# Kernel tuning notes

Measured on AMD Instinct MI355X. Metric: run time of the kernel, lower is better.

The kernel has to match this reference:

```python
import jax, jax.numpy as jnp
import numpy as np

B, L = 2048, 4096
ALPHA = 1.0   # cfgs['metric']['alpha']
BETA = 0.5    # cfgs['metric']['beta']
ENC = 0.0     # cfgs['metric']['enc'] (encoder=None -> term is 0)


def _peak_mask(x, distance):
    """GPU-friendly equivalent of scipy.signal.find_peaks(x, distance=d):
    strict local maxima + min-distance suppression via window-max (NMS).
    x: [B, L] -> bool mask [B, L]."""
    interior = (x[:, 1:-1] > x[:, :-2]) & (x[:, 1:-1] > x[:, 2:])
    local_max = jnp.pad(interior, ((0, 0), (1, 1)))
    w = 2 * distance - 1
    pooled = jax.lax.reduce_window(x, -jnp.inf, jax.lax.max,
                                   (1, w), (1, 1), 'SAME')
    return local_max & (x >= pooled)


def _forward(in_signal, ref_signal):
    # plain MSE over the whole batch
    mse_loss = jnp.mean((in_signal - ref_signal) ** 2)

    # cosine similarity, mean over batch
    dot = jnp.sum(in_signal * ref_signal, axis=-1)
    na = jnp.linalg.norm(in_signal, axis=-1)
    nb = jnp.linalg.norm(ref_signal, axis=-1)
    cosine_similarity = jnp.mean(dot / (na * nb))

    # peak detection: distance=20 for count comparison (custom_error branch)
    m20_in = _peak_mask(in_signal, 20)
    m20_ref = _peak_mask(ref_signal, 20)
    n_in = jnp.sum(m20_in, axis=-1)
    n_ref = jnp.sum(m20_ref, axis=-1)

    # peak-to-peak error: distance=10 peaks; MSE between peak-masked signals
    # (fixed-shape, position-aligned stand-in for get_peaks_info_of_segments)
    m10_in = _peak_mask(in_signal, 10)
    m10_ref = _peak_mask(ref_signal, 10)
    pk_in = jnp.where(m10_in, in_signal, 0.0)
    pk_ref = jnp.where(m10_ref, ref_signal, 0.0)
    p2p_i = jnp.mean((pk_in - pk_ref) ** 2, axis=-1)   # [B]

    mse_i = jnp.mean((in_signal - ref_signal) ** 2, axis=-1)  # [B]

    custom_loss = jnp.sum(jnp.where(n_in != n_ref, mse_i * ALPHA, p2p_i * BETA))
    p2p_loss = jnp.sum(p2p_i)

    total_loss = mse_loss + custom_loss  # + ENC * 0 (encoder is None)
    return jnp.stack([total_loss, cosine_similarity, p2p_loss, mse_loss])


def setup_inputs() -> dict:
    key = jax.random.key(0)
    k1, k2 = jax.random.split(key)
    in_signal = jax.random.normal(k1, (B, L), dtype=jnp.float32)
    ref_signal = jax.random.normal(k2, (B, L), dtype=jnp.float32)
    return {"in_signal": in_signal, "ref_signal": ref_signal}


def reference(in_signal, ref_signal):
    return _forward(in_signal, ref_signal)
```

## Files before the change

### kernel.cpp

```cpp
#include <hip/hip_runtime.h>
#include <math.h>

#define LL 4096
#define BB 2048
#define NT 512
#define CH 8
#define ALPHA 1.0f
#define BETA 0.5f
#define NEG_INF (-__builtin_inff())
#define POS_INF (__builtin_inff())

#define SPSZ 4672
#define OFS(d) ((d) + ((d) >> 3) + 27)

template <int CTRL, int RM>
__device__ __forceinline__ float dpp_addf(float v) {
    int s = __builtin_amdgcn_update_dpp(0, __float_as_int(v), CTRL, RM, 0xf, true);
    return v + __int_as_float(s);
}
__device__ __forceinline__ float wredf(float v) {
    v = dpp_addf<0x111, 0xf>(v);
    v = dpp_addf<0x112, 0xf>(v);
    v = dpp_addf<0x114, 0xf>(v);
    v = dpp_addf<0x118, 0xf>(v);
    v = dpp_addf<0x142, 0xa>(v);
    v = dpp_addf<0x143, 0xc>(v);
    return v;
}

__global__ __launch_bounds__(NT, 6) void row_kernel(const float* __restrict__ gA,
                                                    const float* __restrict__ gB,
                                                    float4* __restrict__ rowout) {
    __shared__ float sS[SPSZ];
    __shared__ float sP[SPSZ];
    __shared__ float4 red4[NT / 64][2];

    const int b = blockIdx.x;
    const int t = threadIdx.x;
    float* const Sb = sS + 9 * t;
    float* const Pb = sP + 9 * t;
    const float* rowA = gA + (size_t)b * LL;
    const float* rowB = gB + (size_t)b * LL;

    float xA[CH], xB[CH];
    {
        const float4* a4 = (const float4*)rowA;
        const float4* b4 = (const float4*)rowB;
#pragma unroll
        for (int k = 0; k < CH / 4; ++k) {
            float4 v = a4[t * (CH / 4) + k];
            xA[4 * k + 0] = v.x; xA[4 * k + 1] = v.y; xA[4 * k + 2] = v.z; xA[4 * k + 3] = v.w;
            float4 u = b4[t * (CH / 4) + k];
            xB[4 * k + 0] = u.x; xB[4 * k + 1] = u.y; xB[4 * k + 2] = u.z; xB[4 * k + 3] = u.w;
        }
    }

    {
        float se = 0.f, dt = 0.f, na = 0.f, nb = 0.f;
#pragma unroll
        for (int j = 0; j < CH; ++j) {
            float d = xA[j] - xB[j];
            se += d * d;
            dt += xA[j] * xB[j];
            na += xA[j] * xA[j];
            nb += xB[j] * xB[j];
        }
        se = wredf(se); dt = wredf(dt); na = wredf(na); nb = wredf(nb);
        if ((t & 63) == 63) red4[t >> 6][0] = make_float4(se, dt, na, nb);
    }

    if (t < 24) {
        int i = t - 24;
        int p = i + (i >> 3) + 27;
        sS[p] = NEG_INF; sP[p] = NEG_INF;
    } else if (t >= NT - 24) {
        int i = LL + (t - (NT - 24));
        int p = i + (i >> 3) + 27;
        sS[p] = NEG_INF; sP[p] = NEG_INF;
    }

    auto process = [&](const float (&x)[CH], int& cnt20, unsigned& m10) {
        float pp[CH], ss[CH];
        pp[0] = x[0];
#pragma unroll
        for (int j = 1; j < CH; ++j) pp[j] = fmaxf(pp[j - 1], x[j]);
        ss[CH - 1] = x[CH - 1];
#pragma unroll
        for (int j = CH - 2; j >= 0; --j) ss[j] = fmaxf(ss[j + 1], x[j]);
#pragma unroll
        for (int j = 0; j < CH; ++j) {
            Pb[j + 27] = pp[j];
            Sb[j + 27] = ss[j];
        }
        const float cmax = pp[CH - 1];
        __syncthreads();

        const float Cm2 = Pb[OFS(-9)];
        const float Cm1 = Pb[OFS(-1)];
        const float Cp1 = Pb[OFS(15)];
        const float Cp2 = Pb[OFS(23)];
        const float f1 = fmaxf(Cm1, cmax);
        const float f2 = fmaxf(cmax, Cp1);
        const float g2 = fmaxf(f1, Cp1);
        const float g1 = fmaxf(g2, Cm2);
        const float g3 = fmaxf(g2, Cp2);
        const float xm1 = (t == 0)      ? POS_INF : Sb[OFS(-1)];
        const float xp1 = (t == NT - 1) ? POS_INF : Pb[OFS(8)];

        cnt20 = 0; m10 = 0u;
#pragma unroll
        for (int j = 0; j < CH; ++j) {
            float xi = x[j];
            float xl = (j > 0)      ? x[j - 1] : xm1;
            float xr = (j < CH - 1) ? x[j + 1] : xp1;
            bool lm = (xi > xl) && (xi > xr);
            float a19 = Sb[OFS(j - 9)];
            float b19 = Pb[OFS(j + 9)];
            float a39 = Sb[OFS(j - 19)];
            float b39 = Pb[OFS(j + 19)];
            float mid19 = (j == 0) ? f1 : ((j == CH - 1) ? f2 : cmax);
            float mid39 = (j <= 2) ? g1 : ((j <= 4) ? g2 : g3);
            float p19 = fmaxf(fmaxf(a19, b19), mid19);
            float p39 = fmaxf(fmaxf(a39, b39), mid39);
            if (lm && xi >= p19) m10 |= (1u << j);
            if (lm && xi >= p39) cnt20++;
        }
    };

    int cntA, cntB;
    unsigned mA, mB;
    process(xA, cntA, mA);
    __syncthreads();
    process(xB, cntB, mB);

    float p2p = 0.f;
#pragma unroll
    for (int j = 0; j < CH; ++j) {
        float av = ((mA >> j) & 1u) ? xA[j] : 0.f;
        float bv = ((mB >> j) & 1u) ? xB[j] : 0.f;
        float d = av - bv;
        p2p += d * d;
    }

    p2p = wredf(p2p);
    float cc = wredf((float)(cntA * 4096 + cntB));
    if ((t & 63) == 63) red4[t >> 6][1] = make_float4(p2p, cc, 0.f, 0.f);
    __syncthreads();

    if (t == 0) {
        float s0 = 0, s1 = 0, s2 = 0, s3 = 0, s4 = 0, s5 = 0;
#pragma unroll
        for (int i = 0; i < NT / 64; ++i) {
            float4 u = red4[i][0];
            float4 v = red4[i][1];
            s0 += u.x; s1 += u.y; s2 += u.z; s3 += u.w;
            s4 += v.x; s5 += v.y;
        }
        int packed = (int)s5;
        int ca = packed >> 12;
        int cb = packed & 4095;
        float mse_i = s0 / (float)LL;
        float cos_i = s1 / (sqrtf(s2) * sqrtf(s3));
        float p2p_i = s4 / (float)LL;
        float custom_i = (ca != cb) ? (mse_i * ALPHA) : (p2p_i * BETA);
        rowout[b] = make_float4(mse_i, cos_i, p2p_i, custom_i);
    }
}

__global__ __launch_bounds__(256) void reduce_kernel(const float4* __restrict__ rows,
                                                     float* __restrict__ out) {
    __shared__ float red[4][4];
    float sx = 0.f, sy = 0.f, sz = 0.f, sw = 0.f;
    for (int r = threadIdx.x; r < BB; r += 256) {
        float4 v = rows[r];
        sx += v.x; sy += v.y; sz += v.z; sw += v.w;
    }
    sx = wredf(sx); sy = wredf(sy); sz = wredf(sz); sw = wredf(sw);
    int w = threadIdx.x >> 6, lane = threadIdx.x & 63;
    if (lane == 63) { red[w][0] = sx; red[w][1] = sy; red[w][2] = sz; red[w][3] = sw; }
    __syncthreads();
    if (threadIdx.x == 0) {
        float ax = 0, ay = 0, az = 0, aw = 0;
        for (int i = 0; i < 4; ++i) {
            ax += red[i][0]; ay += red[i][1]; az += red[i][2]; aw += red[i][3];
        }
        float mse = ax / (float)BB;
        out[0] = mse + aw;
        out[1] = ay / (float)BB;
        out[2] = az;
        out[3] = mse;
    }
}

extern "C" void kernel_launch(void* const* d_in, const int* in_sizes, int n_in,
                              void* d_out, int out_size, void* d_ws, size_t ws_size,
                              hipStream_t stream) {
    const float* inA = (const float*)d_in[0];
    const float* inB = (const float*)d_in[1];
    float* out = (float*)d_out;
    float4* rows = (float4*)d_ws;

    hipLaunchKernelGGL(row_kernel, dim3(BB), dim3(NT), 0, stream, inA, inB, rows);
    hipLaunchKernelGGL(reduce_kernel, dim3(1), dim3(256), 0, stream, rows, out);
}
```

Before: 24.57 us.

## Process each row in two halves with 256 threads and halo-loaded scan tiles

Halves the block to 256 threads and walks each 4096-element row in two 2048-element passes. A small shared buffer holds the prefix/suffix max scans, and the boundary chunks on either side are loaded separately by six halo threads. This replaces the single large whole-row shared buffer. Peak counts are now summed with wave ballots and popcounts instead of a packed float reduction. The smaller shared-memory footprint should allow more resident blocks per CU, at the cost of more barriers and some redundant halo loads.

```diff
diff --git a/kernel.cpp b/kernel.cpp
--- a/kernel.cpp
+++ b/kernel.cpp
@@ -3,15 +3,15 @@
 
 #define LL 4096
 #define BB 2048
-#define NT 512
-#define CH 8
+#define NT 256
+#define NW (NT / 64)
 #define ALPHA 1.0f
 #define BETA 0.5f
 #define NEG_INF (-__builtin_inff())
 #define POS_INF (__builtin_inff())
 
-#define SPSZ 4672
-#define OFS(d) ((d) + ((d) >> 3) + 27)
+#define BSZ (262 * 9)
+#define OFS2(d) (9 * ((d) >> 3) + ((d) & 7))
 
 template <int CTRL, int RM>
 __device__ __forceinline__ float dpp_addf(float v) {
@@ -28,137 +28,151 @@
     return v;
 }
 
-__global__ __launch_bounds__(NT, 6) void row_kernel(const float* __restrict__ gA,
+__global__ __launch_bounds__(NT, 8) void row_kernel(const float* __restrict__ gA,
                                                     const float* __restrict__ gB,
                                                     float4* __restrict__ rowout) {
-    __shared__ float sS[SPSZ];
-    __shared__ float sP[SPSZ];
-    __shared__ float4 red4[NT / 64][2];
+    __shared__ float bS[BSZ];
+    __shared__ float bP[BSZ];
+    __shared__ float4 red4[NW];
+    __shared__ float  redp[NW];
+    __shared__ int    redc[NW][2];
 
     const int b = blockIdx.x;
     const int t = threadIdx.x;
-    float* const Sb = sS + 9 * t;
-    float* const Pb = sP + 9 * t;
     const float* rowA = gA + (size_t)b * LL;
     const float* rowB = gB + (size_t)b * LL;
-
-    float xA[CH], xB[CH];
-    {
-        const float4* a4 = (const float4*)rowA;
-        const float4* b4 = (const float4*)rowB;
-#pragma unroll
-        for (int k = 0; k < CH / 4; ++k) {
-            float4 v = a4[t * (CH / 4) + k];
-            xA[4 * k + 0] = v.x; xA[4 * k + 1] = v.y; xA[4 * k + 2] = v.z; xA[4 * k + 3] = v.w;
-            float4 u = b4[t * (CH / 4) + k];
-            xB[4 * k + 0] = u.x; xB[4 * k + 1] = u.y; xB[4 * k + 2] = u.z; xB[4 * k + 3] = u.w;
-        }
-    }
-
-    {
-        float se = 0.f, dt = 0.f, na = 0.f, nb = 0.f;
-#pragma unroll
-        for (int j = 0; j < CH; ++j) {
-            float d = xA[j] - xB[j];
-            se += d * d;
-            dt += xA[j] * xB[j];
-            na += xA[j] * xA[j];
-            nb += xB[j] * xB[j];
-        }
-        se = wredf(se); dt = wredf(dt); na = wredf(na); nb = wredf(nb);
-        if ((t & 63) == 63) red4[t >> 6][0] = make_float4(se, dt, na, nb);
-    }
-
-    if (t < 24) {
-        int i = t - 24;
-        int p = i + (i >> 3) + 27;
-        sS[p] = NEG_INF; sP[p] = NEG_INF;
-    } else if (t >= NT - 24) {
-        int i = LL + (t - (NT - 24));
-        int p = i + (i >> 3) + 27;
-        sS[p] = NEG_INF; sP[p] = NEG_INF;
-    }
-
-    auto process = [&](const float (&x)[CH], int& cnt20, unsigned& m10) {
-        float pp[CH], ss[CH];
+    float* const Sb = bS + 9 * (t + 3);
+    float* const Pb = bP + 9 * (t + 3);
+    const int kh = (t < 3) ? (t - 3) : (253 + t);
+    float* const Sh = bS + 9 * (kh + 3);
+    float* const Ph = bP + 9 * (kh + 3);
+
+    float se = 0.f, dtp = 0.f, na = 0.f, nb = 0.f, p2p = 0.f;
+    int cntA = 0, cntB = 0;
+
+    auto scan_store = [](const float (&x)[8], float* S, float* P) {
+        float pp[8], ss[8];
         pp[0] = x[0];
 #pragma unroll
-        for (int j = 1; j < CH; ++j) pp[j] = fmaxf(pp[j - 1], x[j]);
-        ss[CH - 1] = x[CH - 1];
-#pragma unroll
-        for (int j = CH - 2; j >= 0; --j) ss[j] = fmaxf(ss[j + 1], x[j]);
-#pragma unroll
-        for (int j = 0; j < CH; ++j) {
-            Pb[j + 27] = pp[j];
-            Sb[j + 27] = ss[j];
-        }
-        const float cmax = pp[CH - 1];
-        __syncthreads();
-
-        const float Cm2 = Pb[OFS(-9)];
-        const float Cm1 = Pb[OFS(-1)];
-        const float Cp1 = Pb[OFS(15)];
-        const float Cp2 = Pb[OFS(23)];
+        for (int j = 1; j < 8; ++j) pp[j] = fmaxf(pp[j - 1], x[j]);
+        ss[7] = x[7];
+#pragma unroll
+        for (int j = 6; j >= 0; --j) ss[j] = fmaxf(ss[j + 1], x[j]);
+#pragma unroll
+        for (int j = 0; j < 8; ++j) { P[j] = pp[j]; S[j] = ss[j]; }
+        return pp[7];
+    };
+
+    auto halo_scan = [&](const float* row, int p) {
+        if (t < 6) {
+            float hx[8];
+            const int gh = 256 * p + kh;
+            if (gh >= 0 && gh < 512) {
+                const float4* h4 = (const float4*)(row + gh * 8);
+                float4 u0 = h4[0], u1 = h4[1];
+                hx[0] = u0.x; hx[1] = u0.y; hx[2] = u0.z; hx[3] = u0.w;
+                hx[4] = u1.x; hx[5] = u1.y; hx[6] = u1.z; hx[7] = u1.w;
+            } else {
+#pragma unroll
+                for (int j = 0; j < 8; ++j) hx[j] = NEG_INF;
+            }
+            scan_store(hx, Sh, Ph);
+        }
+    };
+
+    auto evalsig = [&](const float (&x)[8], float cmax, int p, unsigned& m10, int& cnt) {
+        const float Cm2 = Pb[OFS2(-9)];
+        const float Cm1 = Pb[OFS2(-1)];
+        const float Cp1 = Pb[OFS2(15)];
+        const float Cp2 = Pb[OFS2(23)];
         const float f1 = fmaxf(Cm1, cmax);
         const float f2 = fmaxf(cmax, Cp1);
         const float g2 = fmaxf(f1, Cp1);
         const float g1 = fmaxf(g2, Cm2);
         const float g3 = fmaxf(g2, Cp2);
-        const float xm1 = (t == 0)      ? POS_INF : Sb[OFS(-1)];
-        const float xp1 = (t == NT - 1) ? POS_INF : Pb[OFS(8)];
-
-        cnt20 = 0; m10 = 0u;
-#pragma unroll
-        for (int j = 0; j < CH; ++j) {
+        const float xm1 = (p == 0 && t == 0)      ? POS_INF : Sb[OFS2(-1)];
+        const float xp1 = (p == 1 && t == NT - 1) ? POS_INF : Pb[OFS2(8)];
+        m10 = 0u;
+#pragma unroll
+        for (int j = 0; j < 8; ++j) {
             float xi = x[j];
-            float xl = (j > 0)      ? x[j - 1] : xm1;
-            float xr = (j < CH - 1) ? x[j + 1] : xp1;
+            float xl = (j > 0) ? x[j - 1] : xm1;
+            float xr = (j < 7) ? x[j + 1] : xp1;
             bool lm = (xi > xl) && (xi > xr);
-            float a19 = Sb[OFS(j - 9)];
-            float b19 = Pb[OFS(j + 9)];
-            float a39 = Sb[OFS(j - 19)];
-            float b39 = Pb[OFS(j + 19)];
-            float mid19 = (j == 0) ? f1 : ((j == CH - 1) ? f2 : cmax);
+            float a19 = Sb[OFS2(j - 9)];
+            float b19 = Pb[OFS2(j + 9)];
+            float a39 = Sb[OFS2(j - 19)];
+            float b39 = Pb[OFS2(j + 19)];
+            float mid19 = (j == 0) ? f1 : ((j == 7) ? f2 : cmax);
             float mid39 = (j <= 2) ? g1 : ((j <= 4) ? g2 : g3);
             float p19 = fmaxf(fmaxf(a19, b19), mid19);
             float p39 = fmaxf(fmaxf(a39, b39), mid39);
             if (lm && xi >= p19) m10 |= (1u << j);
-            if (lm && xi >= p39) cnt20++;
+            unsigned long long bal = __ballot(lm && (xi >= p39));
+            cnt += (int)__popcll(bal);
         }
     };
 
-    int cntA, cntB;
-    unsigned mA, mB;
-    process(xA, cntA, mA);
+#pragma unroll
+    for (int p = 0; p < 2; ++p) {
+        const float* rA = rowA + 2048 * p;
+        const float* rB = rowB + 2048 * p;
+        float xA[8], xB[8];
+        {
+            const float4* a4 = (const float4*)rA;
+            const float4* b4 = (const float4*)rB;
+            float4 v0 = a4[2 * t], v1 = a4[2 * t + 1];
+            xA[0] = v0.x; xA[1] = v0.y; xA[2] = v0.z; xA[3] = v0.w;
+            xA[4] = v1.x; xA[5] = v1.y; xA[6] = v1.z; xA[7] = v1.w;
+            float4 u0 = b4[2 * t], u1 = b4[2 * t + 1];
+            xB[0] = u0.x; xB[1] = u0.y; xB[2] = u0.z; xB[3] = u0.w;
+            xB[4] = u1.x; xB[5] = u1.y; xB[6] = u1.z; xB[7] = u1.w;
+        }
+#pragma unroll
+        for (int j = 0; j < 8; ++j) {
+            float d = xA[j] - xB[j];
+            se  += d * d;
+            dtp += xA[j] * xB[j];
+            na  += xA[j] * xA[j];
+            nb  += xB[j] * xB[j];
+        }
+
+        unsigned mA, mB;
+        float cmA = scan_store(xA, Sb, Pb);
+        halo_scan(rowA, p);
+        __syncthreads();
+        evalsig(xA, cmA, p, mA, cntA);
+        __syncthreads();
+        float cmB = scan_store(xB, Sb, Pb);
+        halo_scan(rowB, p);
+        __syncthreads();
+        evalsig(xB, cmB, p, mB, cntB);
+
+#pragma unroll
+        for (int j = 0; j < 8; ++j) {
+            float av = ((mA >> j) & 1u) ? xA[j] : 0.f;
+            float bv = ((mB >> j) & 1u) ? xB[j] : 0.f;
+            float d = av - bv;
+            p2p += d * d;
+        }
+        if (p == 0) __syncthreads();
+    }
+
+    se = wredf(se); dtp = wredf(dtp); na = wredf(na); nb = wredf(nb); p2p = wredf(p2p);
+    const int w = t >> 6;
+    if ((t & 63) == 63) { red4[w] = make_float4(se, dtp, na, nb); redp[w] = p2p; }
+    if ((t & 63) == 0)  { redc[w][0] = cntA; redc[w][1] = cntB; }
     __syncthreads();
-    process(xB, cntB, mB);
-
-    float p2p = 0.f;
-#pragma unroll
-    for (int j = 0; j < CH; ++j) {
-        float av = ((mA >> j) & 1u) ? xA[j] : 0.f;
-        float bv = ((mB >> j) & 1u) ? xB[j] : 0.f;
-        float d = av - bv;
-        p2p += d * d;
-    }
-
-    p2p = wredf(p2p);
-    float cc = wredf((float)(cntA * 4096 + cntB));
-    if ((t & 63) == 63) red4[t >> 6][1] = make_float4(p2p, cc, 0.f, 0.f);
-    __syncthreads();
-
     if (t == 0) {
-        float s0 = 0, s1 = 0, s2 = 0, s3 = 0, s4 = 0, s5 = 0;
-#pragma unroll
-        for (int i = 0; i < NT / 64; ++i) {
-            float4 u = red4[i][0];
-            float4 v = red4[i][1];
+        float s0 = 0, s1 = 0, s2 = 0, s3 = 0, s4 = 0;
+        int ca = 0, cb = 0;
+#pragma unroll
+        for (int i = 0; i < NW; ++i) {
+            float4 u = red4[i];
             s0 += u.x; s1 += u.y; s2 += u.z; s3 += u.w;
-            s4 += v.x; s5 += v.y;
-        }
-        int packed = (int)s5;
-        int ca = packed >> 12;
-        int cb = packed & 4095;
+            s4 += redp[i];
+            ca += redc[i][0]; cb += redc[i][1];
+        }
         float mse_i = s0 / (float)LL;
         float cos_i = s1 / (sqrtf(s2) * sqrtf(s3));
         float p2p_i = s4 / (float)LL;
```

After: 44.38 us. +80.6%, slower.

## Process two rows per block with all global loads issued upfront

Applied to the files above, without the earlier changes.

Each block now handles two rows (b and b+BB/2). It issues all four row loads at kernel start, so the second row's memory traffic overlaps with the first row's compute, and the grid is halved. __syncthreads is replaced by a custom barrier that waits only on LDS counters (lgkmcnt) before s_barrier, so barriers don't stall on outstanding global loads. Register pressure doubles for the input arrays, and with fewer blocks there is less parallelism to hide latency across the GPU.

```diff
diff --git a/kernel.cpp b/kernel.cpp
--- a/kernel.cpp
+++ b/kernel.cpp
@@ -28,6 +28,11 @@
     return v;
 }
 
+__device__ __forceinline__ void barrier_lds() {
+    asm volatile("s_waitcnt lgkmcnt(0)" ::: "memory");
+    __builtin_amdgcn_s_barrier();
+}
+
 __global__ __launch_bounds__(NT, 6) void row_kernel(const float* __restrict__ gA,
                                                     const float* __restrict__ gB,
                                                     float4* __restrict__ rowout) {
@@ -39,34 +44,33 @@
     const int t = threadIdx.x;
     float* const Sb = sS + 9 * t;
     float* const Pb = sP + 9 * t;
-    const float* rowA = gA + (size_t)b * LL;
-    const float* rowB = gB + (size_t)b * LL;
-
-    float xA[CH], xB[CH];
+
+    float x1A[CH], x1B[CH], x2A[CH], x2B[CH];
     {
-        const float4* a4 = (const float4*)rowA;
-        const float4* b4 = (const float4*)rowB;
-#pragma unroll
-        for (int k = 0; k < CH / 4; ++k) {
-            float4 v = a4[t * (CH / 4) + k];
-            xA[4 * k + 0] = v.x; xA[4 * k + 1] = v.y; xA[4 * k + 2] = v.z; xA[4 * k + 3] = v.w;
-            float4 u = b4[t * (CH / 4) + k];
-            xB[4 * k + 0] = u.x; xB[4 * k + 1] = u.y; xB[4 * k + 2] = u.z; xB[4 * k + 3] = u.w;
-        }
-    }
-
-    {
-        float se = 0.f, dt = 0.f, na = 0.f, nb = 0.f;
-#pragma unroll
-        for (int j = 0; j < CH; ++j) {
-            float d = xA[j] - xB[j];
-            se += d * d;
-            dt += xA[j] * xB[j];
-            na += xA[j] * xA[j];
-            nb += xB[j] * xB[j];
-        }
-        se = wredf(se); dt = wredf(dt); na = wredf(na); nb = wredf(nb);
-        if ((t & 63) == 63) red4[t >> 6][0] = make_float4(se, dt, na, nb);
+        const float4* a1 = (const float4*)(gA + (size_t)b * LL);
+        const float4* b1 = (const float4*)(gB + (size_t)b * LL);
+        const float4* a2 = (const float4*)(gA + (size_t)(b + BB / 2) * LL);
+        const float4* b2 = (const float4*)(gB + (size_t)(b + BB / 2) * LL);
+#pragma unroll
+        for (int k = 0; k < CH / 4; ++k) {
+            float4 v = a1[2 * t + k];
+            x1A[4 * k + 0] = v.x; x1A[4 * k + 1] = v.y; x1A[4 * k + 2] = v.z; x1A[4 * k + 3] = v.w;
+        }
+#pragma unroll
+        for (int k = 0; k < CH / 4; ++k) {
+            float4 v = b1[2 * t + k];
+            x1B[4 * k + 0] = v.x; x1B[4 * k + 1] = v.y; x1B[4 * k + 2] = v.z; x1B[4 * k + 3] = v.w;
+        }
+#pragma unroll
+        for (int k = 0; k < CH / 4; ++k) {
+            float4 v = a2[2 * t + k];
+            x2A[4 * k + 0] = v.x; x2A[4 * k + 1] = v.y; x2A[4 * k + 2] = v.z; x2A[4 * k + 3] = v.w;
+        }
+#pragma unroll
+        for (int k = 0; k < CH / 4; ++k) {
+            float4 v = b2[2 * t + k];
+            x2B[4 * k + 0] = v.x; x2B[4 * k + 1] = v.y; x2B[4 * k + 2] = v.z; x2B[4 * k + 3] = v.w;
+        }
     }
 
     if (t < 24) {
@@ -93,7 +97,7 @@
             Sb[j + 27] = ss[j];
         }
         const float cmax = pp[CH - 1];
-        __syncthreads();
+        barrier_lds();
 
         const float Cm2 = Pb[OFS(-9)];
         const float Cm1 = Pb[OFS(-1)];
@@ -127,44 +131,65 @@
         }
     };
 
-    int cntA, cntB;
-    unsigned mA, mB;
-    process(xA, cntA, mA);
-    __syncthreads();
-    process(xB, cntB, mB);
-
-    float p2p = 0.f;
-#pragma unroll
-    for (int j = 0; j < CH; ++j) {
-        float av = ((mA >> j) & 1u) ? xA[j] : 0.f;
-        float bv = ((mB >> j) & 1u) ? xB[j] : 0.f;
-        float d = av - bv;
-        p2p += d * d;
-    }
-
-    p2p = wredf(p2p);
-    float cc = wredf((float)(cntA * 4096 + cntB));
-    if ((t & 63) == 63) red4[t >> 6][1] = make_float4(p2p, cc, 0.f, 0.f);
-    __syncthreads();
-
-    if (t == 0) {
-        float s0 = 0, s1 = 0, s2 = 0, s3 = 0, s4 = 0, s5 = 0;
-#pragma unroll
-        for (int i = 0; i < NT / 64; ++i) {
-            float4 u = red4[i][0];
-            float4 v = red4[i][1];
-            s0 += u.x; s1 += u.y; s2 += u.z; s3 += u.w;
-            s4 += v.x; s5 += v.y;
-        }
-        int packed = (int)s5;
-        int ca = packed >> 12;
-        int cb = packed & 4095;
-        float mse_i = s0 / (float)LL;
-        float cos_i = s1 / (sqrtf(s2) * sqrtf(s3));
-        float p2p_i = s4 / (float)LL;
-        float custom_i = (ca != cb) ? (mse_i * ALPHA) : (p2p_i * BETA);
-        rowout[b] = make_float4(mse_i, cos_i, p2p_i, custom_i);
-    }
+    auto do_row = [&](const float (&xA)[CH], const float (&xB)[CH], int rowIdx) {
+        float se = 0.f, dtp = 0.f, na = 0.f, nb = 0.f;
+#pragma unroll
+        for (int j = 0; j < CH; ++j) {
+            float d = xA[j] - xB[j];
+            se  += d * d;
+            dtp += xA[j] * xB[j];
+            na  += xA[j] * xA[j];
+            nb  += xB[j] * xB[j];
+        }
+
+        int cntA, cntB;
+        unsigned mA, mB;
+        process(xA, cntA, mA);
+        barrier_lds();
+        process(xB, cntB, mB);
+
+        float p2p = 0.f;
+#pragma unroll
+        for (int j = 0; j < CH; ++j) {
+            float av = ((mA >> j) & 1u) ? xA[j] : 0.f;
+            float bv = ((mB >> j) & 1u) ? xB[j] : 0.f;
+            float d = av - bv;
+            p2p += d * d;
+        }
+
+        se = wredf(se); dtp = wredf(dtp); na = wredf(na); nb = wredf(nb);
+        p2p = wredf(p2p);
+        float cc = wredf((float)(cntA * 4096 + cntB));
+        const int w = t >> 6;
+        if ((t & 63) == 63) {
+            red4[w][0] = make_float4(se, dtp, na, nb);
+            red4[w][1] = make_float4(p2p, cc, 0.f, 0.f);
+        }
+        barrier_lds();
+
+        if (t == 0) {
+            float s0 = 0, s1 = 0, s2 = 0, s3 = 0, s4 = 0, s5 = 0;
+#pragma unroll
+            for (int i = 0; i < NT / 64; ++i) {
+                float4 u = red4[i][0];
+                float4 v = red4[i][1];
+                s0 += u.x; s1 += u.y; s2 += u.z; s3 += u.w;
+                s4 += v.x; s5 += v.y;
+            }
+            int packed = (int)s5;
+            int ca = packed >> 12;
+            int cb = packed & 4095;
+            float mse_i = s0 / (float)LL;
+            float cos_i = s1 / (sqrtf(s2) * sqrtf(s3));
+            float p2p_i = s4 / (float)LL;
+            float custom_i = (ca != cb) ? (mse_i * ALPHA) : (p2p_i * BETA);
+            rowout[rowIdx] = make_float4(mse_i, cos_i, p2p_i, custom_i);
+        }
+    };
+
+    do_row(x1A, x1B, b);
+    barrier_lds();
+    do_row(x2A, x2B, b + BB / 2);
 }
 
 __global__ __launch_bounds__(256) void reduce_kernel(const float4* __restrict__ rows,
@@ -200,6 +225,6 @@
     float* out = (float*)d_out;
     float4* rows = (float4*)d_ws;
 
-    hipLaunchKernelGGL(row_kernel, dim3(BB), dim3(NT), 0, stream, inA, inB, rows);
+    hipLaunchKernelGGL(row_kernel, dim3(BB / 2), dim3(NT), 0, stream, inA, inB, rows);
     hipLaunchKernelGGL(reduce_kernel, dim3(1), dim3(256), 0, stream, rows, out);
 }
```

New measurement: 31.18 us. 1.27x slower.
